# Kernel optimization log

Hardware: AMD Instinct MI355X
Metric: run time of the kernel (lower is better)

## Reference

```python
import jax, jax.numpy as jnp
import numpy as np

B, T, C, L = 1024, 256, 100, 64  # batch, time steps, classes (blank=C-1), label length
NEG = -1e30   # safe -inf for log-space DP
EPS = 1e-7    # Keras K.epsilon() added before log


def setup_inputs() -> dict:
    key = jax.random.key(0)
    k1, k2 = jax.random.split(key)
    logits = jax.random.normal(k1, (B, T, C), dtype=jnp.float32)
    y_pred = jax.nn.softmax(logits, axis=-1)  # ctc_batch_cost expects probabilities
    y_true = jax.random.randint(k2, (B, L), 0, C - 1)  # labels in [0, C-2]; blank=C-1
    return {"y_true": y_true, "y_pred": y_pred}


def ctc_loss(y_true, y_pred):
    """Faithful K.ctc_batch_cost with full input/label lengths, blank = C-1."""
    Bb, Tt, Cc = y_pred.shape
    Ll = y_true.shape[1]
    S = 2 * Ll + 1  # extended label lattice: blank-interleaved
    blank = Cc - 1

    # extended labels: [blank, l0, blank, l1, ..., blank]
    ext = jnp.full((Bb, S), blank, dtype=y_true.dtype).at[:, 1::2].set(y_true)
    # skip-transition allowed when ext[s] is non-blank and differs from ext[s-2]
    ext_m2 = jnp.concatenate([jnp.full((Bb, 2), -1, ext.dtype), ext[:, :-2]], axis=1)
    allow = (ext != blank) & (ext != ext_m2)  # [B,S]

    logp = jnp.log(y_pred + EPS)  # [B,T,C]
    # gather log-probs on the lattice once: [B,T,S]
    lp_ext = jnp.take_along_axis(
        logp, jnp.broadcast_to(ext[:, None, :], (Bb, Tt, S)), axis=2)
    lp_seq = jnp.moveaxis(lp_ext, 1, 0)  # [T,B,S] for scan

    # alpha init: only states 0 (blank) and 1 (first label) reachable at t=0
    alpha0 = jnp.where(jnp.arange(S)[None, :] < 2, lp_seq[0], NEG)

    def shift(a, k):
        return jnp.concatenate(
            [jnp.full((Bb, k), NEG, a.dtype), a[:, :-k]], axis=1)

    def step(alpha, lp_t):
        new = jnp.logaddexp(
            jnp.logaddexp(alpha, shift(alpha, 1)),
            jnp.where(allow, shift(alpha, 2), NEG)) + lp_t
        return new, None

    alphaT, _ = jax.lax.scan(step, alpha0, lp_seq[1:])
    # total prob = alpha[T-1, S-1] + alpha[T-1, S-2]
    loss = -jnp.logaddexp(alphaT[:, -1], alphaT[:, -2])
    return loss[:, None]  # ctc_batch_cost returns shape [B,1]


def reference(y_true, y_pred):
    return ctc_loss(y_true, y_pred)
```

## Files before the change

### kernel.cpp

```cpp
#include <hip/hip_runtime.h>

#define B_ 1024
#define T_ 256
#define C_ 100
#define L_ 64
#define EPS_ 1e-7f
#define LN2 0.69314718055994530942f

#define CH 8
#define NCH 16
#define DEPTH 3
#define BROW (T_ * C_ * 4)

#define LOG2F(x) __builtin_amdgcn_logf(x)

typedef const __attribute__((address_space(1))) void GV;
typedef __attribute__((address_space(3))) void LV;

__device__ __forceinline__ void gload_lds16(const void* g, void* l) {
    __builtin_amdgcn_global_load_lds((GV*)g, (LV*)l, 16, 0, 0);
}

__device__ __forceinline__ float dpp_shr1(float x) {
    return __int_as_float(__builtin_amdgcn_update_dpp(
        0, __float_as_int(x), 0x138, 0xf, 0xf, false));
}
__device__ __forceinline__ float dpp_shl1(float x) {
    return __int_as_float(__builtin_amdgcn_update_dpp(
        0, __float_as_int(x), 0x130, 0xf, 0xf, false));
}

#define PLAN(x0_, x1_, x2_) do {                                          \
    float m_ = fmaxf(fmaxf(x0_, x1_), x2_);                               \
    _Pragma("unroll")                                                     \
    for (int d_ = 1; d_ < 64; d_ <<= 1) m_ = fmaxf(m_, __shfl_xor(m_, d_)); \
    const int e_ = (__float_as_int(m_) >> 23) & 255;                      \
    rs_K = 127 - e_;                                                      \
    rs_scale = __int_as_float((254 - e_) << 23);           \
} while (0)

#define APPLY(x0_, x1_, x2_) do { x0_ *= rs_scale; x1_ *= rs_scale;       \
    x2_ *= rs_scale; Sacc += rs_K; } while (0)

#define FSTEP(pb_, pl_) do {                                              \
    const float up1 = dpp_shr1(a1);                                       \
    const float s   = allow ? up1 : 0.0f;                                 \
    const float n0  = (a0 + up1) * (pb_);                                 \
    const float n1  = ((a1 + a0) + s) * (pl_);                            \
    const float n2  = (a2 + a1) * (pb_);                                  \
    a0 = n0; a1 = n1; a2 = n2;                                            \
} while (0)

#define BSTEP(pb_, pl_) do {                                              \
    const float db0 = dpp_shl1(a0);                                       \
    const float db1 = dpp_shl1(a1);                                       \
    const float sc0 = is63 ? a2 : db0;                                    \
    const float sk  = allowN ? db1 : 0.0f;                                \
    const float n0  = (a0 + a1) * (pb_);                                  \
    const float n1  = ((a1 + sc0) + sk) * (pl_);                          \
    const float n2  = a2 * (pb_);                                         \
    a0 = n0; a1 = n1; a2 = n2;                                            \
} while (0)

#define WAITC(c_) do {                                                    \
    if ((c_) <= NCH - 3)      asm volatile("s_waitcnt vmcnt(8)" ::: "memory"); \
    else if ((c_) == NCH - 2) asm volatile("s_waitcnt vmcnt(4)" ::: "memory"); \
    else                      asm volatile("s_waitcnt vmcnt(0)" ::: "memory"); \
} while (0)

#define SISSUE(wv_, c_, off0_) do {                                       \
    _Pragma("unroll")                                                     \
    for (int k_ = 0; k_ < 4; ++k_) {                                      \
        unsigned o_ = (unsigned)(off0_) + k_ * 1024u + ((unsigned)lane << 4); \
        o_ = o_ < (BROW - 16u) ? o_ : (BROW - 16u);                       \
        gload_lds16(bb + o_, &ring[wv_][(c_) & 3][k_ * 256]);             \
    }                                                                     \
} while (0)

__global__ __launch_bounds__(128) void ctc_kernel(
    const int* __restrict__ y_true,
    const float* __restrict__ y_pred,
    float* __restrict__ out)
{
    __shared__ float ring[2][4][1024];
    __shared__ float sG0[64], sG1[64];
    __shared__ float sG2;
    __shared__ int   sSaccB;

    const int tid  = threadIdx.x;
    const int lane = tid & 63;
    const int wv   = tid >> 6;
    const int b    = blockIdx.x;

    const float* __restrict__ base = y_pred + (size_t)b * T_ * C_;
    const char*  __restrict__ bb   = (const char*)base;
    const int  label   = y_true[b * L_ + lane];
    const int  labprev = __shfl_up(label, 1);
    const bool allow   = (lane == 0) || (label != labprev);
    const bool is63    = (lane == 63);
    const bool allowN  = (bool)__shfl_down((int)allow, 1);

    float a0 = 0.0f, a1 = 0.0f, a2 = 0.0f;
    float rs_scale = 1.0f;
    int   rs_K = 0, Sacc = 0;

    if (wv == 0) {
        #pragma unroll
        for (int c = 0; c < DEPTH; ++c) SISSUE(0, c, c * 3200);

        #pragma unroll
        for (int c = 0; c < NCH; ++c) {
            WAITC(c);
            const float* __restrict__ sl = ring[0][c & 3];
            if (c == 0) {
                a0 = (lane == 0) ? (sl[99] + EPS_) : 0.0f;
                a1 = (lane == 0) ? (sl[label] + EPS_) : 0.0f;
                a2 = 0.0f;
                PLAN(a0, a1, a2);
                #pragma unroll
                for (int j = 1; j < CH; ++j)
                    FSTEP(sl[j * 100 + 99] + EPS_, sl[j * 100 + label] + EPS_);
            } else {
                APPLY(a0, a1, a2);
                PLAN(a0, a1, a2);
                #pragma unroll
                for (int j = 0; j < CH; ++j)
                    FSTEP(sl[j * 100 + 99] + EPS_, sl[j * 100 + label] + EPS_);
            }
            if (c + DEPTH < NCH) SISSUE(0, c + DEPTH, (c + DEPTH) * 3200);
        }

        APPLY(a0, a1, a2);
        PLAN(a0, a1, a2);
        APPLY(a0, a1, a2);
    } else {
        #pragma unroll
        for (int c = 0; c < DEPTH; ++c) SISSUE(1, c, 99200 - c * 3200);

        #pragma unroll
        for (int c = 0; c < NCH; ++c) {
            WAITC(c);
            const float* __restrict__ sl = ring[1][c & 3];
            if (c == 0) {
                a2 = sl[799] + EPS_;
                a1 = is63 ? (sl[700 + label] + EPS_) : 0.0f;
                a0 = 0.0f;
                PLAN(a0, a1, a2);
                #pragma unroll
                for (int j = 1; j < CH; ++j)
                    BSTEP(sl[(7 - j) * 100 + 99] + EPS_, sl[(7 - j) * 100 + label] + EPS_);
            } else {
                APPLY(a0, a1, a2);
                PLAN(a0, a1, a2);
                #pragma unroll
                for (int j = 0; j < CH; ++j)
                    BSTEP(sl[(7 - j) * 100 + 99] + EPS_, sl[(7 - j) * 100 + label] + EPS_);
            }
            if (c + DEPTH < NCH) SISSUE(1, c + DEPTH, 99200 - (c + DEPTH) * 3200);
        }

        APPLY(a0, a1, a2);
        PLAN(a0, a1, a2);
        APPLY(a0, a1, a2);

        const float db0 = dpp_shl1(a0);
        const float db1 = dpp_shl1(a1);
        sG0[lane] = a0 + a1;
        sG1[lane] = a1 + (is63 ? a2 : db0) + (allowN ? db1 : 0.0f);
        if (is63) { sG2 = a2; sSaccB = Sacc; }
    }

    __syncthreads();

    if (wv == 0) {
        float prod = a0 * sG0[lane] + a1 * sG1[lane];
        if (is63) prod += a2 * sG2;
        #pragma unroll
        for (int d = 1; d < 64; d <<= 1) prod += __shfl_xor(prod, d);
        if (lane == 0)
            out[b] = -LN2 * (LOG2F(prod) - (float)(Sacc + sSaccB));
    }
}

extern "C" void kernel_launch(void* const* d_in, const int* in_sizes, int n_in,
                              void* d_out, int out_size, void* d_ws, size_t ws_size,
                              hipStream_t stream) {
    const int*   y_true = (const int*)d_in[0];
    const float* y_pred = (const float*)d_in[1];
    float*       out    = (float*)d_out;

    ctc_kernel<<<dim3(B_), dim3(128), 0, stream>>>(y_true, y_pred, out);
}
```

Measured before the change: 23.57 us.

## Replace direct global-to-LDS loads with register-staged loads and double-buffered LDS writes

```diff
diff --git a/kernel.cpp b/kernel.cpp
--- a/kernel.cpp
+++ b/kernel.cpp
@@ -9,17 +9,18 @@
 
 #define CH 8
 #define NCH 16
-#define DEPTH 3
+#define SLOTF 832
 #define BROW (T_ * C_ * 4)
 
 #define LOG2F(x) __builtin_amdgcn_logf(x)
 
-typedef const __attribute__((address_space(1))) void GV;
-typedef __attribute__((address_space(3))) void LV;
-
-__device__ __forceinline__ void gload_lds16(const void* g, void* l) {
-    __builtin_amdgcn_global_load_lds((GV*)g, (LV*)l, 16, 0, 0);
-}
+#define GLD4(dst_, addr_, imm_) \
+    asm volatile("global_load_dwordx4 %0, %1, off offset:" #imm_ \
+                 : "=v"(dst_) : "v"(addr_) : "memory")
+#define GLD1(dst_, addr_) \
+    asm volatile("global_load_dword %0, %1, off" \
+                 : "=v"(dst_) : "v"(addr_) : "memory")
+#define WV(n_) asm volatile("s_waitcnt vmcnt(" #n_ ")" ::: "memory")
 
 __device__ __forceinline__ float dpp_shr1(float x) {
     return __int_as_float(__builtin_amdgcn_update_dpp(
@@ -62,19 +63,36 @@
     a0 = n0; a1 = n1; a2 = n2;                                            \
 } while (0)
 
-#define WAITC(c_) do {                                                    \
-    if ((c_) <= NCH - 3)      asm volatile("s_waitcnt vmcnt(8)" ::: "memory"); \
-    else if ((c_) == NCH - 2) asm volatile("s_waitcnt vmcnt(4)" ::: "memory"); \
-    else                      asm volatile("s_waitcnt vmcnt(0)" ::: "memory"); \
-} while (0)
-
-#define SISSUE(wv_, c_, off0_) do {                                       \
+#define LISSUE(st_, off0_) do {                                           \
+    const char* ap_ = pA + (off0_);                                       \
+    GLD4(sa##st_, ap_, 0);                                                \
+    GLD4(sb##st_, ap_, 1024);                                             \
+    GLD4(sc##st_, ap_, 2048);                                             \
+    unsigned to_ = (unsigned)(off0_) + 3072u + tl4;                       \
+    to_ = to_ < (BROW - 4u) ? to_ : (BROW - 4u);                          \
+    GLD1(sd##st_, bb + to_);                                              \
+} while (0)
+
+#define DSWRITE(st_, slot_) do {                                          \
+    float4* s4_ = (float4*)(slot_);                                       \
+    s4_[lane]       = sa##st_;                                            \
+    s4_[64 + lane]  = sb##st_;                                            \
+    s4_[128 + lane] = sc##st_;                                            \
+    (slot_)[768 + lane] = sd##st_;                                        \
+} while (0)
+
+#define FBODY(sl_) do {                                                   \
+    APPLY(a0, a1, a2); PLAN(a0, a1, a2);                                  \
     _Pragma("unroll")                                                     \
-    for (int k_ = 0; k_ < 4; ++k_) {                                      \
-        unsigned o_ = (unsigned)(off0_) + k_ * 1024u + ((unsigned)lane << 4); \
-        o_ = o_ < (BROW - 16u) ? o_ : (BROW - 16u);                       \
-        gload_lds16(bb + o_, &ring[wv_][(c_) & 3][k_ * 256]);             \
-    }                                                                     \
+    for (int j = 0; j < CH; ++j)                                          \
+        FSTEP((sl_)[j * 100 + 99] + EPS_, (sl_)[j * 100 + label] + EPS_); \
+} while (0)
+
+#define BBODY(sl_) do {                                                   \
+    APPLY(a0, a1, a2); PLAN(a0, a1, a2);                                  \
+    _Pragma("unroll")                                                     \
+    for (int j = 0; j < CH; ++j)                                          \
+        BSTEP((sl_)[(7 - j) * 100 + 99] + EPS_, (sl_)[(7 - j) * 100 + label] + EPS_); \
 } while (0)
 
 __global__ __launch_bounds__(128) void ctc_kernel(
@@ -82,7 +100,7 @@
     const float* __restrict__ y_pred,
     float* __restrict__ out)
 {
-    __shared__ float ring[2][4][1024];
+    __shared__ float ring[2][2][SLOTF];
     __shared__ float sG0[64], sG1[64];
     __shared__ float sG2;
     __shared__ int   sSaccB;
@@ -94,24 +112,43 @@
 
     const float* __restrict__ base = y_pred + (size_t)b * T_ * C_;
     const char*  __restrict__ bb   = (const char*)base;
+    const char*  __restrict__ pA   = bb + ((unsigned)lane << 4);
+    const unsigned tl4 = (unsigned)lane << 2;
+
     const int  label   = y_true[b * L_ + lane];
     const int  labprev = __shfl_up(label, 1);
     const bool allow   = (lane == 0) || (label != labprev);
     const bool is63    = (lane == 63);
     const bool allowN  = (bool)__shfl_down((int)allow, 1);
 
+    float4 sa0, sb0, sc0, sa1, sb1, sc1;
+    float  sd0, sd1;
+
     float a0 = 0.0f, a1 = 0.0f, a2 = 0.0f;
     float rs_scale = 1.0f;
     int   rs_K = 0, Sacc = 0;
 
     if (wv == 0) {
-        #pragma unroll
-        for (int c = 0; c < DEPTH; ++c) SISSUE(0, c, c * 3200);
+        float* __restrict__ s0 = ring[0][0];
+        float* __restrict__ s1 = ring[0][1];
+
+        LISSUE(0, 0u);
+        LISSUE(1, 3200u);
+        WV(4);
+        DSWRITE(0, s0);
+        LISSUE(0, 6400u);
 
         #pragma unroll
         for (int c = 0; c < NCH; ++c) {
-            WAITC(c);
-            const float* __restrict__ sl = ring[0][c & 3];
+            if (c <= 13) { WV(4); } else if (c == 14) { WV(0); }
+            if (c <= 14) {
+                if (((c + 1) & 1) == 0) { DSWRITE(0, s0); } else { DSWRITE(1, s1); }
+            }
+            if (c <= 12) {
+                if (((c + 3) & 1) == 0) { LISSUE(0, (unsigned)(c + 3) * 3200u); }
+                else                    { LISSUE(1, (unsigned)(c + 3) * 3200u); }
+            }
+            const float* __restrict__ sl = (c & 1) ? s1 : s0;
             if (c == 0) {
                 a0 = (lane == 0) ? (sl[99] + EPS_) : 0.0f;
                 a1 = (lane == 0) ? (sl[label] + EPS_) : 0.0f;
@@ -121,26 +158,34 @@
                 for (int j = 1; j < CH; ++j)
                     FSTEP(sl[j * 100 + 99] + EPS_, sl[j * 100 + label] + EPS_);
             } else {
-                APPLY(a0, a1, a2);
-                PLAN(a0, a1, a2);
-                #pragma unroll
-                for (int j = 0; j < CH; ++j)
-                    FSTEP(sl[j * 100 + 99] + EPS_, sl[j * 100 + label] + EPS_);
-            }
-            if (c + DEPTH < NCH) SISSUE(0, c + DEPTH, (c + DEPTH) * 3200);
+                FBODY(sl);
+            }
         }
 
         APPLY(a0, a1, a2);
         PLAN(a0, a1, a2);
         APPLY(a0, a1, a2);
     } else {
-        #pragma unroll
-        for (int c = 0; c < DEPTH; ++c) SISSUE(1, c, 99200 - c * 3200);
+        float* __restrict__ s0 = ring[1][0];
+        float* __restrict__ s1 = ring[1][1];
+
+        LISSUE(0, 99200u);
+        LISSUE(1, 96000u);
+        WV(4);
+        DSWRITE(0, s0);
+        LISSUE(0, 92800u);
 
         #pragma unroll
         for (int c = 0; c < NCH; ++c) {
-            WAITC(c);
-            const float* __restrict__ sl = ring[1][c & 3];
+            if (c <= 13) { WV(4); } else if (c == 14) { WV(0); }
+            if (c <= 14) {
+                if (((c + 1) & 1) == 0) { DSWRITE(0, s0); } else { DSWRITE(1, s1); }
+            }
+            if (c <= 12) {
+                const unsigned o_ = 99200u - (unsigned)(c + 3) * 3200u;
+                if (((c + 3) & 1) == 0) { LISSUE(0, o_); } else { LISSUE(1, o_); }
+            }
+            const float* __restrict__ sl = (c & 1) ? s1 : s0;
             if (c == 0) {
                 a2 = sl[799] + EPS_;
                 a1 = is63 ? (sl[700 + label] + EPS_) : 0.0f;
@@ -150,13 +195,8 @@
                 for (int j = 1; j < CH; ++j)
                     BSTEP(sl[(7 - j) * 100 + 99] + EPS_, sl[(7 - j) * 100 + label] + EPS_);
             } else {
-                APPLY(a0, a1, a2);
-                PLAN(a0, a1, a2);
-                #pragma unroll
-                for (int j = 0; j < CH; ++j)
-                    BSTEP(sl[(7 - j) * 100 + 99] + EPS_, sl[(7 - j) * 100 + label] + EPS_);
-            }
-            if (c + DEPTH < NCH) SISSUE(1, c + DEPTH, 99200 - (c + DEPTH) * 3200);
+                BBODY(sl);
+            }
         }
 
         APPLY(a0, a1, a2);
```

After: 24.46 us. 1.04x slower.
